# Performance work log

Hardware: AMD Instinct MI355X
Metric: run time of the kernel (lower is better)

The kernel has to match this reference:

```python
import jax, jax.numpy as jnp
import numpy as np

N_EMBD = 1024
N_HEAD = 16
B, T = 4, 2048


def setup_inputs() -> dict:
    key = jax.random.key(0)
    ks = jax.random.split(key, 9)
    s = 1.0 / np.sqrt(N_EMBD)
    def lin(k):
        kw, kb = jax.random.split(k)
        W = jax.random.uniform(kw, (N_EMBD, N_EMBD), jnp.float32, -s, s)
        b = jax.random.uniform(kb, (N_EMBD,), jnp.float32, -s, s)
        return W, b
    Wq, bq = lin(ks[0])
    Wk, bk = lin(ks[1])
    Wv, bv = lin(ks[2])
    Wc, bc = lin(ks[3])
    x = jax.random.normal(ks[4], (B, T, N_EMBD), jnp.float32)
    return {"x": x, "Wq": Wq, "bq": bq, "Wk": Wk, "bk": bk,
            "Wv": Wv, "bv": bv, "Wc": Wc, "bc": bc}


def reference(x, Wq, bq, Wk, bk, Wv, bv, Wc, bc):
    Bsz, Tlen, C = x.shape
    hd = C // N_HEAD  # head dim
    # projections (torch Linear: x @ W.T + b)
    q = x @ Wq.T + bq
    k = x @ Wk.T + bk
    v = x @ Wv.T + bv
    # [B, H, T, hd]
    q = q.reshape(Bsz, Tlen, N_HEAD, hd).transpose(0, 2, 1, 3)
    k = k.reshape(Bsz, Tlen, N_HEAD, hd).transpose(0, 2, 1, 3)
    v = v.reshape(Bsz, Tlen, N_HEAD, hd).transpose(0, 2, 1, 3)
    scale = 1.0 / np.sqrt(hd).astype(np.float32)
    att = jnp.einsum('bhqd,bhkd->bhqk', q, k) * scale  # [B,H,T,T]
    causal = jnp.tril(jnp.ones((Tlen, Tlen), dtype=bool))
    att = jnp.where(causal[None, None, :, :], att, -jnp.inf)
    att = jax.nn.softmax(att, axis=-1)
    y = jnp.einsum('bhqk,bhkd->bhqd', att, v)  # [B,H,T,hd]
    y = y.transpose(0, 2, 1, 3).reshape(Bsz, Tlen, C)
    return y @ Wc.T + bc
```

## Files before the change

### kernel.cpp

```cpp
#include <hip/hip_runtime.h>
#include <hip/hip_bf16.h>

typedef __bf16 bf16x8 __attribute__((ext_vector_type(8)));
typedef float f32x4 __attribute__((ext_vector_type(4)));
typedef unsigned short u16;
typedef u16 u16x8 __attribute__((ext_vector_type(8)));
typedef unsigned int u32;
typedef u32 u32x4 __attribute__((ext_vector_type(4)));

#define N_EMBD 1024
#define NH 16
#define HD 64
#define BZ 4
#define TZ 2048
#define QSCALE 0.18033688011f

template<bool B> struct BoolC { static constexpr bool value = B; };

__device__ __forceinline__ u16 f2bf(float f) {
    return __builtin_bit_cast(u16, (__bf16)f);
}

__device__ __forceinline__ void gload16(const void* g, void* l) {
    __builtin_amdgcn_global_load_lds(
        (const __attribute__((address_space(1))) void*)g,
        (__attribute__((address_space(3))) void*)l, 16, 0, 0);
}

__global__ void cvt_f32_bf16(const float* __restrict__ src, u16* __restrict__ dst,
                             int n4, float scale) {
    int i = blockIdx.x * blockDim.x + threadIdx.x;
    if (i < n4) {
        float4 f = ((const float4*)src)[i];
        ushort4 o;
        o.x = f2bf(f.x * scale); o.y = f2bf(f.y * scale);
        o.z = f2bf(f.z * scale); o.w = f2bf(f.w * scale);
        ((ushort4*)dst)[i] = o;
    }
}

__device__ __forceinline__ bf16x8 lds_rd(const u16* base, int row, int g) {
    return *(const bf16x8*)((const char*)base + row * 64 + ((g ^ (row & 3)) << 4));
}

template<int EPI>
__global__ __launch_bounds__(256) void gemm_bt(
    const u16* __restrict__ A, const u16* __restrict__ Bm,
    const float* __restrict__ b0, const float* __restrict__ b1, const float* __restrict__ b2,
    void* __restrict__ Cout, int K) {
    __shared__ __align__(16) u16 Ash[2][128 * 32];
    __shared__ __align__(16) u16 Bsh[2][128 * 32];
    const int tid = threadIdx.x;
    const int lane = tid & 63, wid = tid >> 6;
    const int m0 = blockIdx.x * 128, n0 = blockIdx.y * 128;
    const int wm = wid >> 1, wn = wid & 1;
    f32x4 acc[4][4] = {};

    const int srow = tid >> 2;
    const int scol = ((tid & 3) ^ (srow & 3)) * 8;
    const u16* aA0 = A + (long)(m0 + srow) * K + scol;
    const u16* aA1 = A + (long)(m0 + 64 + srow) * K + scol;
    const u16* aB0 = Bm + (long)(n0 + srow) * K + scol;
    const u16* aB1 = Bm + (long)(n0 + 64 + srow) * K + scol;
    const int ldst = tid * 8;

    const int r = lane & 15, g = lane >> 4;

    auto STAGE = [&](int buf, int kt) {
        gload16(aA0 + kt, &Ash[buf][ldst]);
        gload16(aA1 + kt, &Ash[buf][2048 + ldst]);
        gload16(aB0 + kt, &Bsh[buf][ldst]);
        gload16(aB1 + kt, &Bsh[buf][2048 + ldst]);
    };

    STAGE(0, 0);
    const int nt = K >> 5;
    for (int t = 0; t < nt; ++t) {
        const int cur = t & 1;
        asm volatile("" ::: "memory");
        __builtin_amdgcn_s_barrier();
        asm volatile("" ::: "memory");
        if (t + 1 < nt) {
            STAGE(cur ^ 1, (t + 1) << 5);
            asm volatile("s_waitcnt vmcnt(4)" ::: "memory");
        } else {
            asm volatile("s_waitcnt vmcnt(0)" ::: "memory");
        }
        __builtin_amdgcn_s_barrier();
        asm volatile("" ::: "memory");

        bf16x8 af[4], bfr[4];
#pragma unroll
        for (int m = 0; m < 4; ++m)
            af[m] = lds_rd(Ash[cur], wm * 64 + m * 16 + r, g);
#pragma unroll
        for (int n = 0; n < 4; ++n)
            bfr[n] = lds_rd(Bsh[cur], wn * 64 + n * 16 + r, g);
        __builtin_amdgcn_s_setprio(1);
#pragma unroll
        for (int m = 0; m < 4; ++m)
#pragma unroll
            for (int n = 0; n < 4; ++n)
                acc[m][n] = __builtin_amdgcn_mfma_f32_16x16x32_bf16(af[m], bfr[n], acc[m][n], 0, 0, 0);
        __builtin_amdgcn_s_setprio(0);
    }

    const long planeSz = (long)BZ * NH * TZ * HD;
    if constexpr (EPI == 0) {
        const int proj = n0 >> 10;
        u16* outp = (u16*)Cout;
        if (proj == 2) {
            const int bi = (m0 + wm * 64) >> 11;
#pragma unroll
            for (int n = 0; n < 4; ++n) {
                const int rr = (n0 & 1023) + wn * 64 + n * 16 + r;
                const int h = rr >> 6, d = rr & 63;
                const float bias = b2[rr];
                u16* vcol = outp + 2 * planeSz + (((long)bi * NH + h) * HD + d) * TZ;
#pragma unroll
                for (int m = 0; m < 4; ++m) {
                    const int t0 = (m0 + wm * 64 + m * 16 + g * 4) & 2047;
                    ushort4 o;
                    o.x = f2bf(acc[m][n][0] + bias);
                    o.y = f2bf(acc[m][n][1] + bias);
                    o.z = f2bf(acc[m][n][2] + bias);
                    o.w = f2bf(acc[m][n][3] + bias);
                    *(ushort4*)(vcol + t0) = o;
                }
            }
        } else {
#pragma unroll
            for (int n = 0; n < 4; ++n) {
                const int rr = (n0 & 1023) + wn * 64 + n * 16 + r;
                const int h = rr >> 6, d = rr & 63;
                float bias = (proj == 0 ? b0 : b1)[rr];
                if (proj == 0) bias *= QSCALE;
                const long pbase = (long)proj * planeSz + d;
#pragma unroll
                for (int m = 0; m < 4; ++m)
#pragma unroll
                    for (int reg = 0; reg < 4; ++reg) {
                        const int row = m0 + wm * 64 + m * 16 + g * 4 + reg;
                        const int bi = row >> 11, t = row & 2047;
                        outp[pbase + ((long)bi * NH + h) * (TZ * HD) + (long)t * HD] =
                            f2bf(acc[m][n][reg] + bias);
                    }
            }
        }
    } else {
        float* outp = (float*)Cout;
#pragma unroll
        for (int n = 0; n < 4; ++n) {
            const int col = n0 + wn * 64 + n * 16 + r;
            const float bias = b0[col];
#pragma unroll
            for (int m = 0; m < 4; ++m)
#pragma unroll
                for (int reg = 0; reg < 4; ++reg) {
                    const int row = m0 + wm * 64 + m * 16 + g * 4 + reg;
                    outp[(long)row * N_EMBD + col] = acc[m][n][reg] + bias;
                }
        }
    }
}

__device__ __forceinline__ bf16x8 lds_swz8(const u16* base, int row, int colByte) {
    return *(const bf16x8*)((const char*)base + row * 128 + (colByte ^ ((row & 7) << 4)));
}

__global__ __launch_bounds__(256, 4) void attn_fwd(const u16* __restrict__ qkv, u16* __restrict__ yb) {
    const int i = blockIdx.x;
    const int xcd = i & 7, slot = i >> 3;
    const int bh = xcd + 8 * (slot & 7);
    const int pr = slot >> 3;
    const int b = bh >> 4, h = bh & 15;
    const int tid = threadIdx.x, lane = tid & 63, w = tid >> 6;
    const int r = lane & 15, g = lane >> 4;

    __shared__ __align__(16) u16 Ksh[2][64 * 64];
    __shared__ __align__(16) u16 Vsh[2][64 * 64];

    const long planeSz = (long)BZ * NH * TZ * HD;
    const long bhoff = ((long)b * NH + h) * (long)TZ * HD;
    const u16* qp = qkv + bhoff;
    const u16* kp = qkv + planeSz + bhoff;
    const u16* vTp = qkv + 2 * planeSz + bhoff;

    const int rr8 = tid >> 3, scb = tid & 7;

#pragma unroll 1
    for (int it = 0; it < 2; ++it) {
        const int qblk = it ? pr : (31 - pr);
        const int q0 = qblk * 64;
        const int nkt = qblk + 1;

        bf16x8 qf[2];
        {
            const int q = q0 + w * 16 + r;
#pragma unroll
            for (int ks = 0; ks < 2; ++ks)
                qf[ks] = *(const bf16x8*)(qp + (long)q * HD + ks * 32 + g * 8);
        }

        f32x4 yacc[4] = {};
        float mrun = -__builtin_inff(), lpart = 0.f;

#pragma unroll
        for (int h2 = 0; h2 < 2; ++h2) {
            const int kk = h2 * 32 + rr8;
            const int ss = (scb ^ (kk & 7)) * 8;
            gload16(kp + (long)kk * HD + ss, &Ksh[0][h2 * 2048 + tid * 8]);
            gload16(vTp + (long)kk * TZ + ss, &Vsh[0][h2 * 2048 + tid * 8]);
        }

        auto tile = [&](int kt, auto maskc) {
            constexpr bool MASK = decltype(maskc)::value;
            const int cur = kt & 1;
            const int k0 = kt * 64;
            if (kt + 1 < nkt) {
                const int k0n = k0 + 64;
#pragma unroll
                for (int h2 = 0; h2 < 2; ++h2) {
                    const int kk = h2 * 32 + rr8;
                    const int ss = (scb ^ (kk & 7)) * 8;
                    gload16(kp + (long)(k0n + kk) * HD + ss, &Ksh[cur ^ 1][h2 * 2048 + tid * 8]);
                    gload16(vTp + (long)kk * TZ + k0n + ss, &Vsh[cur ^ 1][h2 * 2048 + tid * 8]);
                }
                asm volatile("s_waitcnt vmcnt(4)" ::: "memory");
            } else {
                asm volatile("s_waitcnt vmcnt(0)" ::: "memory");
            }
            __builtin_amdgcn_s_barrier();
            asm volatile("" ::: "memory");

            f32x4 sac[4] = {};
#pragma unroll
            for (int ks = 0; ks < 2; ++ks) {
                bf16x8 kf[4];
#pragma unroll
                for (int nk = 0; nk < 4; ++nk)
                    kf[nk] = lds_swz8(Ksh[cur], nk * 16 + r, ks * 64 + g * 16);
                __builtin_amdgcn_s_setprio(1);
#pragma unroll
                for (int nk = 0; nk < 4; ++nk)
                    sac[nk] = __builtin_amdgcn_mfma_f32_16x16x32_bf16(kf[nk], qf[ks], sac[nk], 0, 0, 0);
                __builtin_amdgcn_s_setprio(0);
            }

            if constexpr (MASK) {
                const int q = q0 + w * 16 + r;
#pragma unroll
                for (int nk = 0; nk < 4; ++nk)
#pragma unroll
                    for (int reg = 0; reg < 4; ++reg) {
                        const int k = k0 + nk * 16 + g * 4 + reg;
                        sac[nk][reg] = (k > q) ? -__builtin_inff() : sac[nk][reg];
                    }
            }
            float pmax;
            {
                float t0 = fmaxf(fmaxf(sac[0][0], sac[0][1]), fmaxf(sac[0][2], sac[0][3]));
                float t1 = fmaxf(fmaxf(sac[1][0], sac[1][1]), fmaxf(sac[1][2], sac[1][3]));
                float t2 = fmaxf(fmaxf(sac[2][0], sac[2][1]), fmaxf(sac[2][2], sac[2][3]));
                float t3 = fmaxf(fmaxf(sac[3][0], sac[3][1]), fmaxf(sac[3][2], sac[3][3]));
                pmax = fmaxf(fmaxf(t0, t1), fmaxf(t2, t3));
            }
            if (__any(pmax > mrun + 8.0f)) {
                float mx = pmax;
                mx = fmaxf(mx, __shfl_xor(mx, 16));
                mx = fmaxf(mx, __shfl_xor(mx, 32));
                const float mnew = fmaxf(mrun, mx);
                const float corr = __builtin_amdgcn_exp2f(mrun - mnew);
                lpart *= corr;
#pragma unroll
                for (int nd = 0; nd < 4; ++nd)
                    yacc[nd] *= corr;
                mrun = mnew;
            }
            float rs[4];
#pragma unroll
            for (int nk = 0; nk < 4; ++nk) {
                float p0 = __builtin_amdgcn_exp2f(sac[nk][0] - mrun);
                float p1 = __builtin_amdgcn_exp2f(sac[nk][1] - mrun);
                float p2 = __builtin_amdgcn_exp2f(sac[nk][2] - mrun);
                float p3 = __builtin_amdgcn_exp2f(sac[nk][3] - mrun);
                sac[nk][0] = p0; sac[nk][1] = p1;
                sac[nk][2] = p2; sac[nk][3] = p3;
                rs[nk] = (p0 + p1) + (p2 + p3);
            }
            lpart += (rs[0] + rs[1]) + (rs[2] + rs[3]);

            u32 wv[4][2];
#pragma unroll
            for (int nk = 0; nk < 4; ++nk)
#pragma unroll
                for (int j2 = 0; j2 < 2; ++j2)
                    asm("v_cvt_pk_bf16_f32 %0, %1, %2"
                        : "=v"(wv[nk][j2])
                        : "v"(sac[nk][2 * j2]), "v"(sac[nk][2 * j2 + 1]));
            u32 pw[2][4];
#pragma unroll
            for (int ks = 0; ks < 2; ++ks) {
                u32 a0 = wv[2 * ks][0], b0 = wv[2 * ks + 1][0];
                u32 a1 = wv[2 * ks][1], b1 = wv[2 * ks + 1][1];
                asm("v_permlane32_swap_b32 %0, %1" : "+v"(a0), "+v"(b0));
                asm("v_permlane32_swap_b32 %0, %1" : "+v"(a1), "+v"(b1));
                asm("v_permlane16_swap_b32 %0, %1" : "+v"(a0), "+v"(b0));
                asm("v_permlane16_swap_b32 %0, %1" : "+v"(a1), "+v"(b1));
                pw[ks][0] = a0; pw[ks][1] = a1;
                pw[ks][2] = b0; pw[ks][3] = b1;
            }

#pragma unroll
            for (int ks = 0; ks < 2; ++ks) {
                bf16x8 vf[4];
#pragma unroll
                for (int nd = 0; nd < 4; ++nd)
                    vf[nd] = lds_swz8(Vsh[cur], nd * 16 + r, ks * 64 + g * 16);
                const u32x4 pwv = { pw[ks][0], pw[ks][1], pw[ks][2], pw[ks][3] };
                const bf16x8 pb = __builtin_bit_cast(bf16x8, pwv);
                __builtin_amdgcn_s_setprio(1);
#pragma unroll
                for (int nd = 0; nd < 4; ++nd)
                    yacc[nd] = __builtin_amdgcn_mfma_f32_16x16x32_bf16(vf[nd], pb, yacc[nd], 0, 0, 0);
                __builtin_amdgcn_s_setprio(0);
            }

            asm volatile("" ::: "memory");
            __builtin_amdgcn_s_barrier();
            asm volatile("" ::: "memory");
        };

        for (int kt = 0; kt < nkt - 1; ++kt) tile(kt, BoolC<false>{});
        tile(nkt - 1, BoolC<true>{});

        {
            float l = lpart;
            l += __shfl_xor(l, 16);
            l += __shfl_xor(l, 32);
            const float inv = 1.f / l;
            const int q = q0 + w * 16 + r;
            u16* orow = yb + ((long)b * TZ + q) * N_EMBD + h * HD;
#pragma unroll
            for (int nd = 0; nd < 4; ++nd) {
                ushort4 o;
                o.x = f2bf(yacc[nd][0] * inv);
                o.y = f2bf(yacc[nd][1] * inv);
                o.z = f2bf(yacc[nd][2] * inv);
                o.w = f2bf(yacc[nd][3] * inv);
                *(ushort4*)(orow + nd * 16 + g * 4) = o;
            }
        }
    }
}

extern "C" void kernel_launch(void* const* d_in, const int* in_sizes, int n_in,
                              void* d_out, int out_size, void* d_ws, size_t ws_size,
                              hipStream_t stream) {
    const float* x  = (const float*)d_in[0];
    const float* Wq = (const float*)d_in[1];
    const float* bq = (const float*)d_in[2];
    const float* Wk = (const float*)d_in[3];
    const float* bk = (const float*)d_in[4];
    const float* Wv = (const float*)d_in[5];
    const float* bv = (const float*)d_in[6];
    const float* Wc = (const float*)d_in[7];
    const float* bc = (const float*)d_in[8];

    char* ws = (char*)d_ws;
    u16* xb   = (u16*)(ws);
    u16* wqkv = (u16*)(ws + 16777216);
    u16* wcb  = (u16*)(ws + 23068672);
    u16* qkv  = (u16*)(ws + 25165824);
    u16* yb   = (u16*)(ws + 75497472);

    cvt_f32_bf16<<<8192, 256, 0, stream>>>(x, xb, 2097152, 1.0f);
    cvt_f32_bf16<<<1024, 256, 0, stream>>>(Wq, wqkv, 262144, QSCALE);
    cvt_f32_bf16<<<1024, 256, 0, stream>>>(Wk, wqkv + 1048576, 262144, 1.0f);
    cvt_f32_bf16<<<1024, 256, 0, stream>>>(Wv, wqkv + 2097152, 262144, 1.0f);
    cvt_f32_bf16<<<1024, 256, 0, stream>>>(Wc, wcb, 262144, 1.0f);

    gemm_bt<0><<<dim3(64, 24), 256, 0, stream>>>(xb, wqkv, bq, bk, bv, (void*)qkv, 1024);

    attn_fwd<<<1024, 256, 0, stream>>>(qkv, yb);

    gemm_bt<1><<<dim3(64, 8), 256, 0, stream>>>(yb, wcb, bc, nullptr, nullptr, d_out, 1024);
}
```

Baseline: 183.7 us.

## Enlarge GEMM tiles to 256x256 with 8 waves and phased LDS pipeline

Replaces the 128x128, 4-wave GEMM with a 256x256 tile run by 8 waves. Each wave now holds an 8x4 grid of MFMA accumulators, and K advances in 64-wide steps split into two halves. A finer phased schedule interleaves partial global->LDS staging with the MFMA quarters across double-buffered slots and uses a new XOR swizzle. The aim is better operand reuse and overlap of loads with compute. The trade-off is fewer blocks: 384 for the QKV GEMM and only 128 for the output projection, which may underfill the GPU's CUs, plus higher register and LDS pressure.

```diff
diff --git a/kernel.cpp b/kernel.cpp
--- a/kernel.cpp
+++ b/kernel.cpp
@@ -39,78 +39,110 @@
     }
 }
 
-__device__ __forceinline__ bf16x8 lds_rd(const u16* base, int row, int g) {
-    return *(const bf16x8*)((const char*)base + row * 64 + ((g ^ (row & 3)) << 4));
-}
-
 template<int EPI>
-__global__ __launch_bounds__(256) void gemm_bt(
+__global__ __launch_bounds__(512, 2) void gemm_bt(
     const u16* __restrict__ A, const u16* __restrict__ Bm,
     const float* __restrict__ b0, const float* __restrict__ b1, const float* __restrict__ b2,
     void* __restrict__ Cout, int K) {
-    __shared__ __align__(16) u16 Ash[2][128 * 32];
-    __shared__ __align__(16) u16 Bsh[2][128 * 32];
+    __shared__ __align__(16) u16 Ash[2][2][8192];
+    __shared__ __align__(16) u16 Bsh[2][2][8192];
+
     const int tid = threadIdx.x;
     const int lane = tid & 63, wid = tid >> 6;
-    const int m0 = blockIdx.x * 128, n0 = blockIdx.y * 128;
-    const int wm = wid >> 1, wn = wid & 1;
-    f32x4 acc[4][4] = {};
-
-    const int srow = tid >> 2;
-    const int scol = ((tid & 3) ^ (srow & 3)) * 8;
-    const u16* aA0 = A + (long)(m0 + srow) * K + scol;
-    const u16* aA1 = A + (long)(m0 + 64 + srow) * K + scol;
-    const u16* aB0 = Bm + (long)(n0 + srow) * K + scol;
-    const u16* aB1 = Bm + (long)(n0 + 64 + srow) * K + scol;
+    const int wm = wid >> 2, wn = wid & 3;
+    const int m0 = blockIdx.x * 256, n0 = blockIdx.y * 256;
+    const int r = lane & 15, g = lane >> 4;
+
+    f32x4 acc[8][4] = {};
+
+    const int p0 = tid >> 3;
+    const int ci = tid & 7;
+    const int cl = ci ^ (p0 & 7);
+    const int trow = 2 * p0 + (cl >> 2);
+    const int colb = (cl & 3) * 8;
+    const u16* aS = A + (long)(m0 + trow) * K + colb;
+    const u16* bS = Bm + (long)(n0 + trow) * K + colb;
+    const long rowskip = (long)128 * K;
     const int ldst = tid * 8;
 
-    const int r = lane & 15, g = lane >> 4;
-
-    auto STAGE = [&](int buf, int kt) {
-        gload16(aA0 + kt, &Ash[buf][ldst]);
-        gload16(aA1 + kt, &Ash[buf][2048 + ldst]);
-        gload16(aB0 + kt, &Bsh[buf][ldst]);
-        gload16(aB1 + kt, &Bsh[buf][2048 + ldst]);
+    auto STAGE_A = [&](int slot, int kh, int kt) {
+        const u16* sp = aS + kt * 64 + kh * 32;
+        gload16(sp, &Ash[slot][kh][ldst]);
+        gload16(sp + rowskip, &Ash[slot][kh][4096 + ldst]);
     };
-
-    STAGE(0, 0);
-    const int nt = K >> 5;
-    for (int t = 0; t < nt; ++t) {
-        const int cur = t & 1;
-        asm volatile("" ::: "memory");
-        __builtin_amdgcn_s_barrier();
-        asm volatile("" ::: "memory");
-        if (t + 1 < nt) {
-            STAGE(cur ^ 1, (t + 1) << 5);
-            asm volatile("s_waitcnt vmcnt(4)" ::: "memory");
-        } else {
-            asm volatile("s_waitcnt vmcnt(0)" ::: "memory");
-        }
-        __builtin_amdgcn_s_barrier();
-        asm volatile("" ::: "memory");
-
-        bf16x8 af[4], bfr[4];
-#pragma unroll
-        for (int m = 0; m < 4; ++m)
-            af[m] = lds_rd(Ash[cur], wm * 64 + m * 16 + r, g);
-#pragma unroll
-        for (int n = 0; n < 4; ++n)
-            bfr[n] = lds_rd(Bsh[cur], wn * 64 + n * 16 + r, g);
-        __builtin_amdgcn_s_setprio(1);
-#pragma unroll
-        for (int m = 0; m < 4; ++m)
-#pragma unroll
-            for (int n = 0; n < 4; ++n)
-                acc[m][n] = __builtin_amdgcn_mfma_f32_16x16x32_bf16(af[m], bfr[n], acc[m][n], 0, 0, 0);
-        __builtin_amdgcn_s_setprio(0);
+    auto STAGE_B = [&](int slot, int kh, int kt) {
+        const u16* sp = bS + kt * 64 + kh * 32;
+        gload16(sp, &Bsh[slot][kh][ldst]);
+        gload16(sp + rowskip, &Bsh[slot][kh][4096 + ldst]);
+    };
+
+    const int xa = (((((r & 1) << 2) | g) ^ (r >> 1)) << 4);
+    const int arow0 = wm * 64 + (r >> 1);
+    const int brow0 = wn * 32 + (r >> 1);
+    auto RD = [&](const u16* base, int prow) -> bf16x8 {
+        return *(const bf16x8*)((const char*)base + prow * 128 + xa);
+    };
+
+    bf16x8 bfr[4];
+
+#define PHASE(S, KH, QM, STG, ENDW)                                              \
+    {                                                                            \
+        bf16x8 af[4];                                                            \
+        _Pragma("unroll")                                                        \
+        for (int m = 0; m < 4; ++m)                                              \
+            af[m] = RD(&Ash[S][KH][0], arow0 + QM * 32 + m * 8);                 \
+        if (QM == 0) {                                                           \
+            _Pragma("unroll")                                                    \
+            for (int n = 0; n < 4; ++n)                                          \
+                bfr[n] = RD(&Bsh[S][KH][0], brow0 + n * 8);                      \
+        }                                                                        \
+        STG;                                                                     \
+        __builtin_amdgcn_s_barrier();                                            \
+        asm volatile("s_waitcnt lgkmcnt(0)" ::: "memory");                       \
+        __builtin_amdgcn_s_setprio(1);                                           \
+        _Pragma("unroll")                                                        \
+        for (int m = 0; m < 4; ++m)                                              \
+            _Pragma("unroll")                                                    \
+            for (int n = 0; n < 4; ++n)                                          \
+                acc[QM * 4 + m][n] = __builtin_amdgcn_mfma_f32_16x16x32_bf16(    \
+                    af[m], bfr[n], acc[QM * 4 + m][n], 0, 0, 0);                 \
+        __builtin_amdgcn_s_setprio(0);                                           \
+        if (ENDW) asm volatile("s_waitcnt vmcnt(8)" ::: "memory");               \
+        asm volatile("" ::: "memory");                                           \
+        __builtin_amdgcn_s_barrier();                                            \
+        asm volatile("" ::: "memory");                                           \
     }
+
+    STAGE_A(0, 0, 0); STAGE_B(0, 0, 0);
+    STAGE_A(0, 1, 0); STAGE_B(0, 1, 0);
+    STAGE_A(1, 0, 1); STAGE_B(1, 0, 1);
+    asm volatile("s_waitcnt vmcnt(8)" ::: "memory");
+    __builtin_amdgcn_s_barrier();
+    asm volatile("" ::: "memory");
+
+    const int nt = K >> 6;
+    for (int tt = 0; tt < nt; tt += 2) {
+        const int kt1 = tt + 1;
+        const int kt2 = (tt + 2 < nt) ? tt + 2 : 0;
+        const int kt3 = (tt + 3 < nt) ? tt + 3 : 0;
+        PHASE(0, 0, 0, STAGE_A(1, 1, kt1), 0)
+        PHASE(0, 0, 1, STAGE_B(1, 1, kt1), 1)
+        PHASE(0, 1, 0, STAGE_A(0, 0, kt2), 0)
+        PHASE(0, 1, 1, STAGE_B(0, 0, kt2), 1)
+        PHASE(1, 0, 0, STAGE_A(0, 1, kt2), 0)
+        PHASE(1, 0, 1, STAGE_B(0, 1, kt2), 1)
+        PHASE(1, 1, 0, STAGE_A(1, 0, kt3), 0)
+        PHASE(1, 1, 1, STAGE_B(1, 0, kt3), 1)
+    }
+#undef PHASE
+    asm volatile("s_waitcnt vmcnt(0)" ::: "memory");
 
     const long planeSz = (long)BZ * NH * TZ * HD;
     if constexpr (EPI == 0) {
         const int proj = n0 >> 10;
         u16* outp = (u16*)Cout;
         if (proj == 2) {
-            const int bi = (m0 + wm * 64) >> 11;
+            const int bi = (m0 + wm * 128) >> 11;
 #pragma unroll
             for (int n = 0; n < 4; ++n) {
                 const int rr = (n0 & 1023) + wn * 64 + n * 16 + r;
@@ -118,13 +150,13 @@
                 const float bias = b2[rr];
                 u16* vcol = outp + 2 * planeSz + (((long)bi * NH + h) * HD + d) * TZ;
 #pragma unroll
-                for (int m = 0; m < 4; ++m) {
-                    const int t0 = (m0 + wm * 64 + m * 16 + g * 4) & 2047;
+                for (int mf = 0; mf < 8; ++mf) {
+                    const int t0 = (m0 + wm * 128 + mf * 16 + g * 4) & 2047;
                     ushort4 o;
-                    o.x = f2bf(acc[m][n][0] + bias);
-                    o.y = f2bf(acc[m][n][1] + bias);
-                    o.z = f2bf(acc[m][n][2] + bias);
-                    o.w = f2bf(acc[m][n][3] + bias);
+                    o.x = f2bf(acc[mf][n][0] + bias);
+                    o.y = f2bf(acc[mf][n][1] + bias);
+                    o.z = f2bf(acc[mf][n][2] + bias);
+                    o.w = f2bf(acc[mf][n][3] + bias);
                     *(ushort4*)(vcol + t0) = o;
                 }
             }
@@ -137,13 +169,13 @@
                 if (proj == 0) bias *= QSCALE;
                 const long pbase = (long)proj * planeSz + d;
 #pragma unroll
-                for (int m = 0; m < 4; ++m)
+                for (int mf = 0; mf < 8; ++mf)
 #pragma unroll
                     for (int reg = 0; reg < 4; ++reg) {
-                        const int row = m0 + wm * 64 + m * 16 + g * 4 + reg;
+                        const int row = m0 + wm * 128 + mf * 16 + g * 4 + reg;
                         const int bi = row >> 11, t = row & 2047;
                         outp[pbase + ((long)bi * NH + h) * (TZ * HD) + (long)t * HD] =
-                            f2bf(acc[m][n][reg] + bias);
+                            f2bf(acc[mf][n][reg] + bias);
                     }
             }
         }
@@ -154,11 +186,11 @@
             const int col = n0 + wn * 64 + n * 16 + r;
             const float bias = b0[col];
 #pragma unroll
-            for (int m = 0; m < 4; ++m)
+            for (int mf = 0; mf < 8; ++mf)
 #pragma unroll
                 for (int reg = 0; reg < 4; ++reg) {
-                    const int row = m0 + wm * 64 + m * 16 + g * 4 + reg;
-                    outp[(long)row * N_EMBD + col] = acc[m][n][reg] + bias;
+                    const int row = m0 + wm * 128 + mf * 16 + g * 4 + reg;
+                    outp[(long)row * N_EMBD + col] = acc[mf][n][reg] + bias;
                 }
         }
     }
@@ -380,9 +412,9 @@
     cvt_f32_bf16<<<1024, 256, 0, stream>>>(Wv, wqkv + 2097152, 262144, 1.0f);
     cvt_f32_bf16<<<1024, 256, 0, stream>>>(Wc, wcb, 262144, 1.0f);
 
-    gemm_bt<0><<<dim3(64, 24), 256, 0, stream>>>(xb, wqkv, bq, bk, bv, (void*)qkv, 1024);
+    gemm_bt<0><<<dim3(32, 12), 512, 0, stream>>>(xb, wqkv, bq, bk, bv, (void*)qkv, 1024);
 
     attn_fwd<<<1024, 256, 0, stream>>>(qkv, yb);
 
-    gemm_bt<1><<<dim3(64, 8), 256, 0, stream>>>(yb, wcb, bc, nullptr, nullptr, d_out, 1024);
-}
+    gemm_bt<1><<<dim3(32, 4), 512, 0, stream>>>(yb, wcb, bc, nullptr, nullptr, d_out, 1024);
+}
```

Result: no change. 185.4 us (+0.9%).

## Rework GEMM into 256x128 tiles with six-stage LDS pipeline and 512 threads

Applied to the files above, without the earlier changes.

The bf16 projection GEMM now uses 256x128 block tiles with 8 waves and a six-buffer ring of direct-to-LDS loads, so several K-tiles stay in flight. Fragment reads for the next K-step are double-buffered in registers so they overlap the current MFMAs, and there is one barrier per K-step. The LDS layout packs two 32-wide rows into each 128-byte row with a new XOR swizzle. The goal is to hide global memory latency and raise MFMA utilisation. The cost is more LDS per block and more register pressure, and launch_bounds(512,2) constrains occupancy.

```diff
diff --git a/kernel.cpp b/kernel.cpp
--- a/kernel.cpp
+++ b/kernel.cpp
@@ -39,71 +39,106 @@
     }
 }
 
-__device__ __forceinline__ bf16x8 lds_rd(const u16* base, int row, int g) {
-    return *(const bf16x8*)((const char*)base + row * 64 + ((g ^ (row & 3)) << 4));
-}
-
 template<int EPI>
-__global__ __launch_bounds__(256) void gemm_bt(
+__global__ __launch_bounds__(512, 2) void gemm_bt(
     const u16* __restrict__ A, const u16* __restrict__ Bm,
     const float* __restrict__ b0, const float* __restrict__ b1, const float* __restrict__ b2,
     void* __restrict__ Cout, int K) {
-    __shared__ __align__(16) u16 Ash[2][128 * 32];
-    __shared__ __align__(16) u16 Bsh[2][128 * 32];
+    __shared__ __align__(16) u16 Ash[6 * 8192];
+    __shared__ __align__(16) u16 Bsh[6 * 4096];
+
     const int tid = threadIdx.x;
     const int lane = tid & 63, wid = tid >> 6;
-    const int m0 = blockIdx.x * 128, n0 = blockIdx.y * 128;
     const int wm = wid >> 1, wn = wid & 1;
+    const int m0 = blockIdx.x * 256, n0 = blockIdx.y * 128;
+    const int r = lane & 15, g = lane >> 4;
+
     f32x4 acc[4][4] = {};
 
-    const int srow = tid >> 2;
-    const int scol = ((tid & 3) ^ (srow & 3)) * 8;
-    const u16* aA0 = A + (long)(m0 + srow) * K + scol;
-    const u16* aA1 = A + (long)(m0 + 64 + srow) * K + scol;
-    const u16* aB0 = Bm + (long)(n0 + srow) * K + scol;
-    const u16* aB1 = Bm + (long)(n0 + 64 + srow) * K + scol;
+    const int p0 = tid >> 3;
+    const int ci = tid & 7;
+    const int cl = ci ^ (p0 & 7);
+    const int trow = 2 * p0 + (cl >> 2);
+    const int colb = (cl & 3) * 8;
+    const u16* aS = A + (long)(m0 + trow) * K + colb;
+    const u16* bS = Bm + (long)(n0 + trow) * K + colb;
+    const long rowskip = (long)128 * K;
     const int ldst = tid * 8;
 
-    const int r = lane & 15, g = lane >> 4;
-
-    auto STAGE = [&](int buf, int kt) {
-        gload16(aA0 + kt, &Ash[buf][ldst]);
-        gload16(aA1 + kt, &Ash[buf][2048 + ldst]);
-        gload16(aB0 + kt, &Bsh[buf][ldst]);
-        gload16(aB1 + kt, &Bsh[buf][2048 + ldst]);
+    auto STAGE = [&](int sig, int kq) {
+        const u16* spA = aS + kq * 32;
+        gload16(spA, &Ash[sig * 8192 + ldst]);
+        gload16(spA + rowskip, &Ash[sig * 8192 + 4096 + ldst]);
+        gload16(bS + kq * 32, &Bsh[sig * 4096 + ldst]);
     };
 
-    STAGE(0, 0);
-    const int nt = K >> 5;
-    for (int t = 0; t < nt; ++t) {
-        const int cur = t & 1;
+    const int xa = (((((r & 1) << 2) | g) ^ (r >> 1)) << 4);
+    const int arow0 = wm * 32 + (r >> 1);
+    const int brow0 = wn * 32 + (r >> 1);
+    auto RD = [&](const u16* base, int prow) -> bf16x8 {
+        return *(const bf16x8*)((const char*)base + prow * 128 + xa);
+    };
+
+    bf16x8 fa0[4], fb0[4], fa1[4], fb1[4];
+
+    auto READF = [&](int rho, bf16x8* fa, bf16x8* fb) {
+#pragma unroll
+        for (int m = 0; m < 4; ++m) fa[m] = RD(&Ash[rho * 8192], arow0 + m * 8);
+#pragma unroll
+        for (int n = 0; n < 4; ++n) fb[n] = RD(&Bsh[rho * 4096], brow0 + n * 8);
+    };
+    auto MM = [&](bf16x8* fa, bf16x8* fb) {
+        __builtin_amdgcn_s_setprio(1);
+#pragma unroll
+        for (int m = 0; m < 4; ++m)
+#pragma unroll
+            for (int n = 0; n < 4; ++n)
+                acc[m][n] = __builtin_amdgcn_mfma_f32_16x16x32_bf16(fa[m], fb[n], acc[m][n], 0, 0, 0);
+        __builtin_amdgcn_s_setprio(0);
+    };
+    auto BAR = [&] {
         asm volatile("" ::: "memory");
         __builtin_amdgcn_s_barrier();
         asm volatile("" ::: "memory");
-        if (t + 1 < nt) {
-            STAGE(cur ^ 1, (t + 1) << 5);
-            asm volatile("s_waitcnt vmcnt(4)" ::: "memory");
-        } else {
-            asm volatile("s_waitcnt vmcnt(0)" ::: "memory");
-        }
-        __builtin_amdgcn_s_barrier();
-        asm volatile("" ::: "memory");
-
-        bf16x8 af[4], bfr[4];
-#pragma unroll
-        for (int m = 0; m < 4; ++m)
-            af[m] = lds_rd(Ash[cur], wm * 64 + m * 16 + r, g);
-#pragma unroll
-        for (int n = 0; n < 4; ++n)
-            bfr[n] = lds_rd(Bsh[cur], wn * 64 + n * 16 + r, g);
-        __builtin_amdgcn_s_setprio(1);
-#pragma unroll
-        for (int m = 0; m < 4; ++m)
-#pragma unroll
-            for (int n = 0; n < 4; ++n)
-                acc[m][n] = __builtin_amdgcn_mfma_f32_16x16x32_bf16(af[m], bfr[n], acc[m][n], 0, 0, 0);
-        __builtin_amdgcn_s_setprio(0);
+    };
+
+    const int nph = K >> 5;
+
+    STAGE(0, 0); STAGE(1, 1); STAGE(2, 2); STAGE(3, 3); STAGE(4, 4);
+    asm volatile("s_waitcnt vmcnt(9)" ::: "memory");
+    BAR();
+    READF(0, fa0, fb0);
+
+    int rho = 0;
+    for (int p = 0; p + 2 < nph; p += 2) {
+        const int rho1 = rho + 1;
+        const int rho2 = (rho + 2 == 6) ? 0 : rho + 2;
+        const int sigE = (rho == 0) ? 5 : rho - 1;
+        const int kqE = (p + 5 < nph) ? p + 5 : 0;
+        const int kqO = (p + 6 < nph) ? p + 6 : 0;
+        BAR();
+        READF(rho1, fa1, fb1);
+        STAGE(sigE, kqE);
+        MM(fa0, fb0);
+        asm volatile("s_waitcnt vmcnt(9)" ::: "memory");
+        BAR();
+        READF(rho2, fa0, fb0);
+        STAGE(rho, kqO);
+        MM(fa1, fb1);
+        asm volatile("s_waitcnt vmcnt(9)" ::: "memory");
+        rho = rho2;
     }
+    {
+        const int rho1 = rho + 1;
+        const int sigE = (rho == 0) ? 5 : rho - 1;
+        BAR();
+        READF(rho1, fa1, fb1);
+        STAGE(sigE, 0);
+        MM(fa0, fb0);
+        asm volatile("s_waitcnt vmcnt(9)" ::: "memory");
+    }
+    MM(fa1, fb1);
+    asm volatile("s_waitcnt vmcnt(0)" ::: "memory");
 
     const long planeSz = (long)BZ * NH * TZ * HD;
     if constexpr (EPI == 0) {
@@ -380,9 +415,9 @@
     cvt_f32_bf16<<<1024, 256, 0, stream>>>(Wv, wqkv + 2097152, 262144, 1.0f);
     cvt_f32_bf16<<<1024, 256, 0, stream>>>(Wc, wcb, 262144, 1.0f);
 
-    gemm_bt<0><<<dim3(64, 24), 256, 0, stream>>>(xb, wqkv, bq, bk, bv, (void*)qkv, 1024);
+    gemm_bt<0><<<dim3(32, 24), 512, 0, stream>>>(xb, wqkv, bq, bk, bv, (void*)qkv, 1024);
 
     attn_fwd<<<1024, 256, 0, stream>>>(qkv, yb);
 
-    gemm_bt<1><<<dim3(64, 8), 256, 0, stream>>>(yb, wcb, bc, nullptr, nullptr, d_out, 1024);
-}
+    gemm_bt<1><<<dim3(32, 8), 512, 0, stream>>>(yb, wcb, bc, nullptr, nullptr, d_out, 1024);
+}
```

New measurement: 169.4 us. 1.08x faster.
